# Performance work log

Hardware: AMD Instinct MI355X
Metric: run time of the kernel (lower is better)

## Reference

```python
import jax, jax.numpy as jnp
import numpy as np

N, D, H, O, E, K = 16384, 512, 512, 64, 8, 2


def _layernorm(x, g, b, eps=1e-5):
    mu = jnp.mean(x, axis=-1, keepdims=True)
    var = jnp.var(x, axis=-1, keepdims=True)
    return (x - mu) * jax.lax.rsqrt(var + eps) * g + b


def _gelu(x):
    return jax.nn.gelu(x, approximate=False)  # torch nn.GELU default (erf)


def setup_inputs() -> dict:
    key = jax.random.key(0)
    ks = jax.random.split(key, 20)
    s = 0.02
    return {
        "x": jax.random.normal(ks[0], (N, D), jnp.float32),
        # gate: Linear(D,H) -> LN(H) -> GELU -> Linear(H,E)
        "g_w1": jax.random.normal(ks[1], (D, H), jnp.float32) * s,
        "g_b1": jnp.zeros((H,), jnp.float32),
        "g_ln_g": jnp.ones((H,), jnp.float32),
        "g_ln_b": jnp.zeros((H,), jnp.float32),
        "g_w2": jax.random.normal(ks[2], (H, E), jnp.float32) * s,
        "g_b2": jnp.zeros((E,), jnp.float32),
        # experts (stacked over E): Linear(D,H)+LN+GELU, Linear(H,H)+LN+GELU, Linear(H,O)
        "e_w1": jax.random.normal(ks[3], (E, D, H), jnp.float32) * s,
        "e_b1": jnp.zeros((E, H), jnp.float32),
        "e_ln1_g": jnp.ones((E, H), jnp.float32),
        "e_ln1_b": jnp.zeros((E, H), jnp.float32),
        "e_w2": jax.random.normal(ks[4], (E, H, H), jnp.float32) * s,
        "e_b2": jnp.zeros((E, H), jnp.float32),
        "e_ln2_g": jnp.ones((E, H), jnp.float32),
        "e_ln2_b": jnp.zeros((E, H), jnp.float32),
        "e_w3": jax.random.normal(ks[5], (E, H, O), jnp.float32) * s,
        "e_b3": jnp.zeros((E, O), jnp.float32),
        # output projection Linear(O,O)
        "p_w": jax.random.normal(ks[6], (O, O), jnp.float32) * s,
        "p_b": jnp.zeros((O,), jnp.float32),
    }


def reference(x, g_w1, g_b1, g_ln_g, g_ln_b, g_w2, g_b2,
              e_w1, e_b1, e_ln1_g, e_ln1_b, e_w2, e_b2, e_ln2_g, e_ln2_b,
              e_w3, e_b3, p_w, p_b):
    n = x.shape[0]
    # --- gate ---
    gh = _gelu(_layernorm(x @ g_w1 + g_b1, g_ln_g, g_ln_b))
    gate_logits = gh @ g_w2 + g_b2                      # [N, E]
    gate_weights = jax.nn.softmax(gate_logits, axis=-1)
    top_k_weights, top_k_indices = jax.lax.top_k(gate_weights, K)
    top_k_weights = top_k_weights / jnp.sum(top_k_weights, axis=-1, keepdims=True)
    # dense per-token expert weights [N, E] (sum of top-k weights routed to each expert)
    w_dense = jnp.zeros((n, e_w1.shape[0]), x.dtype).at[
        jnp.arange(n)[:, None], top_k_indices].add(top_k_weights)
    # --- all experts on all tokens (faithful to dense loop) ---
    h1 = _gelu(_layernorm(jnp.einsum('nd,edh->enh', x, e_w1) + e_b1[:, None, :],
                          e_ln1_g[:, None, :], e_ln1_b[:, None, :]))
    h2 = _gelu(_layernorm(jnp.einsum('enh,ehk->enk', h1, e_w2) + e_b2[:, None, :],
                          e_ln2_g[:, None, :], e_ln2_b[:, None, :]))
    expert_out = jnp.einsum('enh,eho->eno', h2, e_w3) + e_b3[:, None, :]  # [E, N, O]
    combined = jnp.einsum('ne,eno->no', w_dense, expert_out)              # [N, O]
    output = combined @ p_w + p_b
    expert_usage = jnp.mean(gate_weights, axis=0)
    return (output, gate_weights, top_k_indices, top_k_weights, expert_usage)
```

## Files before the change

kernel.cpp:

```cpp
#include <hip/hip_runtime.h>
#include <hip/hip_bf16.h>

#define N_TOK 16384
#define MAX_SLOTS 33280
#define MAX_BLOCKS 520

typedef __attribute__((ext_vector_type(8))) short bf16x8;
typedef __attribute__((ext_vector_type(4))) float f32x4;
typedef unsigned short u16;

__device__ __forceinline__ u16 f2bf(float f) {
  __hip_bfloat16 h = __float2bfloat16(f);
  union { __hip_bfloat16 b; u16 u; } c; c.b = h; return c.u;
}
__device__ __forceinline__ float bfbits2f(u16 u) {
  return __uint_as_float(((unsigned)u) << 16);
}
__device__ __forceinline__ float gelu_erf(float x) {
  return 0.5f * x * (1.0f + erff(x * 0.70710678118654752f));
}
__device__ __forceinline__ float gelu_fast(float x) {
  float u = x * (0.79788456f + 0.035677408f * x * x);
  float ex;
  asm("v_exp_f32 %0, %1" : "=v"(ex) : "v"(-2.8853901f * u));
  float den = 1.0f + ex;
  float r;
  asm("v_rcp_f32 %0, %1" : "=v"(r) : "v"(den));
  return x * r;
}
__device__ __forceinline__ void gload16(const u16* g, char* lds) {
  __builtin_amdgcn_global_load_lds(
      (const __attribute__((address_space(1))) void*)g,
      (__attribute__((address_space(3))) void*)lds, 16, 0, 0);
}

__global__ __launch_bounds__(256) void prep_x(const float* __restrict__ x,
                                              u16* __restrict__ xbf,
                                              u16* __restrict__ xlo) {
  size_t i = (size_t)blockIdx.x * 256 + threadIdx.x;
  float4 v = ((const float4*)x)[i];
  float a[4] = {v.x, v.y, v.z, v.w};
  union { u16 us[4]; unsigned long long ll; } hb, lb;
#pragma unroll
  for (int j = 0; j < 4; ++j) {
    u16 hu = f2bf(a[j]);
    hb.us[j] = hu;
    lb.us[j] = f2bf(a[j] - bfbits2f(hu));
  }
  *(unsigned long long*)(xbf + i * 4) = hb.ll;
  *(unsigned long long*)(xlo + i * 4) = lb.ll;
}

template <int C>
__global__ __launch_bounds__(256) void pack_w(const float* __restrict__ src,
                                              u16* __restrict__ dst, int R) {
  __shared__ float tl[64][65];
  const int e = blockIdx.z;
  const int k0 = blockIdx.x * 64, n0 = blockIdx.y * 64;
  const float* s = src + (size_t)e * R * C;
  const int tr = threadIdx.x >> 2;
  const int tc4 = (threadIdx.x & 3) * 16;
#pragma unroll
  for (int j = 0; j < 4; ++j) {
    float4 v = *(const float4*)(s + (size_t)(k0 + tr) * C + n0 + tc4 + j * 4);
    tl[tr][tc4 + j * 4 + 0] = v.x;
    tl[tr][tc4 + j * 4 + 1] = v.y;
    tl[tr][tc4 + j * 4 + 2] = v.z;
    tl[tr][tc4 + j * 4 + 3] = v.w;
  }
  __syncthreads();
  const int nl = threadIdx.x >> 2;
  const int kl = (threadIdx.x & 3) * 16;
  const int n = n0 + nl;
  const int sx = (n >> 1) & 3;
  const int t = (k0 + kl) >> 5;
  const int q0 = ((k0 + kl) & 31) >> 3;
#pragma unroll
  for (int c = 0; c < 2; ++c) {
    int q = q0 + c;
    int p = q ^ sx;
    union { u16 us[8]; unsigned long long ll[2]; } o;
#pragma unroll
    for (int j = 0; j < 8; ++j) o.us[j] = f2bf(tl[kl + c * 8 + j][nl]);
    u16* d = dst + (((size_t)e * (R / 32) + t) * C + n) * 32 + p * 8;
    ((unsigned long long*)d)[0] = o.ll[0];
    ((unsigned long long*)d)[1] = o.ll[1];
  }
}

__global__ __launch_bounds__(256) void prep_wcat(const float* __restrict__ gw1,
                                                 u16* __restrict__ wp) {
  int idx = blockIdx.x * 256 + threadIdx.x;
  int p = idx & 3;
  int n = (idx >> 2) & 511;
  int t = idx >> 11;
  int q = p ^ ((n >> 1) & 3);
  int k0 = t * 32 + q * 8;
  union { u16 us[8]; unsigned long long ll[2]; } o;
#pragma unroll
  for (int j = 0; j < 8; ++j) {
    int k = k0 + j;
    u16 v;
    if (k < 512) {
      v = f2bf(gw1[k * 512 + n]);
    } else if (k < 1024) {
      float w = gw1[(k - 512) * 512 + n];
      v = f2bf(w - bfbits2f(f2bf(w)));
    } else {
      v = f2bf(gw1[(k - 1024) * 512 + n]);
    }
    o.us[j] = v;
  }
  unsigned long long* d = (unsigned long long*)(wp + (size_t)idx * 8);
  d[0] = o.ll[0];
  d[1] = o.ll[1];
}

__global__ __launch_bounds__(256) void prep_w2t(const float* __restrict__ gw2,
                                                float* __restrict__ w2t) {
  int i = blockIdx.x * 256 + threadIdx.x;
  int e = i >> 9, k = i & 511;
  w2t[i] = gw2[k * 8 + e];
}

template <int ROUTED, int GATHER, int LNOUT, int FAST>
__global__ __launch_bounds__(512, 4) void gemm_core(
    const u16* __restrict__ A, const u16* __restrict__ A2,
    const u16* __restrict__ Wp, long w_estride, int klen, long osplit,
    const float* __restrict__ bias, int b_estride,
    const float* __restrict__ lng, const float* __restrict__ lnb,
    u16* __restrict__ outb, float* __restrict__ outf,
    const int* __restrict__ slot_token, const int* __restrict__ blk_e,
    const int* __restrict__ blk_tok0) {
  constexpr int ABYTES = 4096;
  constexpr int BUF = ABYTES + 32768;
  constexpr int TSU = 16384;
  extern __shared__ char smem[];

  const int tid = threadIdx.x;
  const int lane = tid & 63;
  const int wv = tid >> 6;
  const int wn = wv * 64;
  const int l15 = lane & 15;
  const int lk = lane >> 4;
  const int swzk16 = (lk ^ ((l15 >> 1) & 3)) << 4;

  int e, row0, kt0, kbase;
  if (ROUTED) {
    e = blk_e[blockIdx.x];
    if (e < 0) return;
    row0 = blk_tok0[blockIdx.x];
    kt0 = 0; kbase = 0;
  } else {
    e = 0;
    row0 = blockIdx.x * 64;
    kbase = blockIdx.y * klen;
    kt0 = kbase >> 5;
  }
  const u16* We = Wp + (size_t)e * w_estride;

  const int lrq = lane >> 2;
  const int cse = (((lane & 3) ^ ((lane >> 3) & 3)) << 3);
  size_t off[5];
  int ldsoff[5], typ[5];
#pragma unroll
  for (int i = 0; i < 5; ++i) {
    int id = wv + 8 * i;
    if (id >= 36) { typ[i] = 2; off[i] = 0; ldsoff[i] = 0; continue; }
    if (id < 4) {
      int lr = id * 16 + lrq;
      long grow = GATHER ? (long)slot_token[row0 + lr] : (long)(row0 + lr);
      off[i] = (size_t)grow * 512 + cse;
      ldsoff[i] = id * 1024 + lane * 16;
      typ[i] = 0;
    } else {
      int bg = id - 4;
      off[i] = (size_t)bg * 512 + lane * 8;
      ldsoff[i] = ABYTES + bg * 1024 + lane * 16;
      typ[i] = 1;
    }
  }

  auto STAGE = [&](int t, char* b) {
    const int kg = kbase + t * 32;
    const u16* Aseg = A;
    int kc = kg;
    if (A2) {
      if (kg >= 1024) { Aseg = A2; kc = kg - 1024; }
      else if (kg >= 512) kc = kg - 512;
    }
    const u16* Bt = We + (size_t)(kt0 + t) * TSU;
#pragma unroll
    for (int i = 0; i < 5; ++i) {
      if (typ[i] == 0)      gload16(Aseg + off[i] + kc, b + ldsoff[i]);
      else if (typ[i] == 1) gload16(Bt + off[i], b + ldsoff[i]);
    }
  };

  f32x4 acc[4][4];
#pragma unroll
  for (int i = 0; i < 4; ++i)
#pragma unroll
    for (int j = 0; j < 4; ++j) acc[i][j] = (f32x4){0.f, 0.f, 0.f, 0.f};

  const int nt = klen / 32;
  char* buf0 = smem;
  char* buf1 = smem + BUF;

  STAGE(0, buf0);
  __syncthreads();
  for (int t = 0; t < nt; ++t) {
    char* cur = (t & 1) ? buf1 : buf0;
    char* nxt = (t & 1) ? buf0 : buf1;
    if (t + 1 < nt) STAGE(t + 1, nxt);
    char* cB = cur + ABYTES;
    bf16x8 af[4];
#pragma unroll
    for (int fm = 0; fm < 4; ++fm)
      af[fm] = *(const bf16x8*)(cur + (fm * 16 + l15) * 64 + swzk16);
#pragma unroll
    for (int fn = 0; fn < 4; ++fn) {
      bf16x8 bv = *(const bf16x8*)(cB + (wn + fn * 16 + l15) * 64 + swzk16);
#pragma unroll
      for (int fm = 0; fm < 4; ++fm)
        acc[fm][fn] = __builtin_amdgcn_mfma_f32_16x16x32_bf16(
            af[fm], bv, acc[fm][fn], 0, 0, 0);
    }
    __syncthreads();
  }

  if constexpr (LNOUT) {
    const float* be = bias + (size_t)e * b_estride;
    const float* ge = lng + (size_t)e * b_estride;
    const float* bbe = lnb + (size_t)e * b_estride;
    float bias_v[4], g_v[4], b_v[4];
#pragma unroll
    for (int fn = 0; fn < 4; ++fn) {
      int col = wn + fn * 16 + l15;
      bias_v[fn] = be[col]; g_v[fn] = ge[col]; b_v[fn] = bbe[col];
    }
#pragma unroll
    for (int fm = 0; fm < 4; ++fm)
#pragma unroll
      for (int fn = 0; fn < 4; ++fn)
#pragma unroll
        for (int r = 0; r < 4; ++r) acc[fm][fn][r] += bias_v[fn];

    float* redS1 = (float*)smem;
    float* redS2 = redS1 + 8 * 64;
#pragma unroll
    for (int fm = 0; fm < 4; ++fm)
#pragma unroll
      for (int r = 0; r < 4; ++r) {
        float a1 = 0.f, a2 = 0.f;
#pragma unroll
        for (int fn = 0; fn < 4; ++fn) {
          float v = acc[fm][fn][r];
          a1 += v; a2 += v * v;
        }
#pragma unroll
        for (int m = 1; m < 16; m <<= 1) {
          a1 += __shfl_xor(a1, m, 64);
          a2 += __shfl_xor(a2, m, 64);
        }
        if (l15 == 0) {
          int row = fm * 16 + lk * 4 + r;
          redS1[wv * 64 + row] = a1;
          redS2[wv * 64 + row] = a2;
        }
      }
    __syncthreads();
#pragma unroll
    for (int fm = 0; fm < 4; ++fm)
#pragma unroll
      for (int r = 0; r < 4; ++r) {
        int row = fm * 16 + lk * 4 + r;
        float S1 = 0.f, S2 = 0.f;
#pragma unroll
        for (int q = 0; q < 8; ++q) {
          S1 += redS1[q * 64 + row];
          S2 += redS2[q * 64 + row];
        }
        float mu = S1 * (1.0f / 512.0f);
        float var = S2 * (1.0f / 512.0f) - mu * mu;
        float rs = rsqrtf(var + 1e-5f);
        size_t rowg = (size_t)(row0 + row);
#pragma unroll
        for (int fn = 0; fn < 4; ++fn) {
          int col = wn + fn * 16 + l15;
          float v = (acc[fm][fn][r] - mu) * rs * g_v[fn] + b_v[fn];
          v = FAST ? gelu_fast(v) : gelu_erf(v);
          outb[rowg * 512 + col] = f2bf(v);
        }
      }
  } else {
    float* dst = outf + (size_t)blockIdx.y * osplit;
#pragma unroll
    for (int fm = 0; fm < 4; ++fm)
#pragma unroll
      for (int r = 0; r < 4; ++r) {
        size_t rowg = (size_t)(row0 + fm * 16 + lk * 4 + r);
#pragma unroll
        for (int fn = 0; fn < 4; ++fn)
          dst[rowg * 512 + wn + fn * 16 + l15] = acc[fm][fn][r];
      }
  }
}

__global__ __launch_bounds__(256) void gate2_topk(
    const float* __restrict__ gh0, const float* __restrict__ gh1,
    const float* __restrict__ b1, const float* __restrict__ lng,
    const float* __restrict__ lnb, const float* __restrict__ w2t,
    const float* __restrict__ b2, float* __restrict__ gwout,
    float* __restrict__ idxout, float* __restrict__ tkwout) {
  const int lane = threadIdx.x & 63;
  const int wv = threadIdx.x >> 6;
  const int t = blockIdx.x * 4 + wv;
  const int c0 = lane * 8;
  float v[8];
  {
    float4 a0 = *(const float4*)(gh0 + (size_t)t * 512 + c0);
    float4 a1 = *(const float4*)(gh0 + (size_t)t * 512 + c0 + 4);
    float4 h0 = *(const float4*)(gh1 + (size_t)t * 512 + c0);
    float4 h1 = *(const float4*)(gh1 + (size_t)t * 512 + c0 + 4);
    float4 bb0 = *(const float4*)(b1 + c0);
    float4 bb1 = *(const float4*)(b1 + c0 + 4);
    v[0] = a0.x + h0.x + bb0.x; v[1] = a0.y + h0.y + bb0.y;
    v[2] = a0.z + h0.z + bb0.z; v[3] = a0.w + h0.w + bb0.w;
    v[4] = a1.x + h1.x + bb1.x; v[5] = a1.y + h1.y + bb1.y;
    v[6] = a1.z + h1.z + bb1.z; v[7] = a1.w + h1.w + bb1.w;
  }
  float s1 = 0.f, s2 = 0.f;
#pragma unroll
  for (int j = 0; j < 8; ++j) { s1 += v[j]; s2 += v[j] * v[j]; }
#pragma unroll
  for (int m = 1; m < 64; m <<= 1) {
    s1 += __shfl_xor(s1, m, 64);
    s2 += __shfl_xor(s2, m, 64);
  }
  float mu = s1 * (1.0f / 512.0f);
  float var = s2 * (1.0f / 512.0f) - mu * mu;
  float rs = rsqrtf(var + 1e-5f);
  float y[8];
  {
    float4 g0 = *(const float4*)(lng + c0);
    float4 g1 = *(const float4*)(lng + c0 + 4);
    float4 q0 = *(const float4*)(lnb + c0);
    float4 q1 = *(const float4*)(lnb + c0 + 4);
    float gg[8] = {g0.x, g0.y, g0.z, g0.w, g1.x, g1.y, g1.z, g1.w};
    float qq[8] = {q0.x, q0.y, q0.z, q0.w, q1.x, q1.y, q1.z, q1.w};
#pragma unroll
    for (int j = 0; j < 8; ++j)
      y[j] = gelu_erf((v[j] - mu) * rs * gg[j] + qq[j]);
  }
  float logit[8];
#pragma unroll
  for (int e = 0; e < 8; ++e) {
    const float4* wr = (const float4*)(w2t + e * 512 + c0);
    float4 w0 = wr[0], w1 = wr[1];
    float p = y[0] * w0.x + y[1] * w0.y + y[2] * w0.z + y[3] * w0.w +
              y[4] * w1.x + y[5] * w1.y + y[6] * w1.z + y[7] * w1.w;
#pragma unroll
    for (int m = 1; m < 64; m <<= 1) p += __shfl_xor(p, m, 64);
    logit[e] = p + b2[e];
  }
  if (lane == 0) {
    float mx = logit[0];
#pragma unroll
    for (int e = 1; e < 8; ++e) mx = fmaxf(mx, logit[e]);
    float w[8], ssum = 0.f;
#pragma unroll
    for (int e = 0; e < 8; ++e) { w[e] = expf(logit[e] - mx); ssum += w[e]; }
    float inv = 1.0f / ssum;
#pragma unroll
    for (int e = 0; e < 8; ++e) w[e] *= inv;
    float w1v = -1.f, w2v = -1.f; int i1 = 0, i2 = 0;
#pragma unroll
    for (int e = 0; e < 8; ++e) {
      float vv = w[e];
      if (vv > w1v)      { w2v = w1v; i2 = i1; w1v = vv; i1 = e; }
      else if (vv > w2v) { w2v = vv; i2 = e; }
    }
    float s = w1v + w2v;
#pragma unroll
    for (int e = 0; e < 8; ++e) gwout[t * 8 + e] = w[e];
    idxout[t * 2] = (float)i1; idxout[t * 2 + 1] = (float)i2;
    tkwout[t * 2] = w1v / s;   tkwout[t * 2 + 1] = w2v / s;
  }
}

__global__ __launch_bounds__(256) void usage_k(const float* __restrict__ gw,
                                               float* __restrict__ usage) {
  __shared__ float r[256];
  int e = blockIdx.x;
  float s = 0.f;
  for (int t = threadIdx.x; t < N_TOK; t += 256) s += gw[t * 8 + e];
  r[threadIdx.x] = s;
  __syncthreads();
  for (int st = 128; st > 0; st >>= 1) {
    if (threadIdx.x < st) r[threadIdx.x] += r[threadIdx.x + st];
    __syncthreads();
  }
  if (threadIdx.x == 0) usage[e] = r[0] * (1.0f / (float)N_TOK);
}

__global__ __launch_bounds__(256) void count_hist(const float* __restrict__ idxout,
                                                  int* __restrict__ blk_cnt) {
  __shared__ int h[8];
  if (threadIdx.x < 8) h[threadIdx.x] = 0;
  __syncthreads();
  int t = blockIdx.x * 256 + threadIdx.x;
  int e0 = (int)idxout[t * 2], e1 = (int)idxout[t * 2 + 1];
  atomicAdd(&h[e0], 1);
  atomicAdd(&h[e1], 1);
  __syncthreads();
  if (threadIdx.x < 8) blk_cnt[blockIdx.x * 8 + threadIdx.x] = h[threadIdx.x];
}

__global__ __launch_bounds__(512) void k_offsets2(
    const int* __restrict__ blk_cnt, int* __restrict__ sbase,
    int* __restrict__ blk_e, int* __restrict__ blk_tok0) {
  __shared__ int cnt[64][8];
  __shared__ int ecnt[8];
  __shared__ int offs[8];
  const int tid = threadIdx.x;
  cnt[tid >> 3][tid & 7] = blk_cnt[tid];
  __syncthreads();
  if (tid < 8) {
    int s = 0;
    for (int b = 0; b < 64; ++b) s += cnt[b][tid];
    ecnt[tid] = s;
  }
  __syncthreads();
  if (tid == 0) {
    int off = 0;
    for (int e = 0; e < 8; ++e) {
      offs[e] = off;
      off += ((ecnt[e] + 63) >> 6) << 6;
    }
  }
  __syncthreads();
  {
    int b = tid >> 3, e = tid & 7;
    int s = offs[e];
    for (int bp = 0; bp < b; ++bp) s += cnt[bp][e];
    sbase[tid] = s;
  }
  for (int b = tid; b < MAX_BLOCKS; b += 512) {
    int acc = 0, be = -1, bt = 0;
#pragma unroll
    for (int e = 0; e < 8; ++e) {
      int nbe = (ecnt[e] + 63) >> 6;
      if (b >= acc && b < acc + nbe) { be = e; bt = offs[e] + (b - acc) * 64; }
      acc += nbe;
    }
    blk_e[b] = be;
    blk_tok0[b] = bt;
  }
}

__global__ __launch_bounds__(256) void k_padinit(int* __restrict__ slot_token,
                                                 float* __restrict__ slot_w) {
  int i = blockIdx.x * 256 + threadIdx.x;
  if (i < MAX_SLOTS) { slot_token[i] = 0; slot_w[i] = 0.f; }
}

__global__ __launch_bounds__(256) void k_scatter2(
    const float* __restrict__ idxout, const float* __restrict__ tkwout,
    const int* __restrict__ sbase, int* __restrict__ slot_token,
    float* __restrict__ slot_w, int* __restrict__ tok_slot) {
  __shared__ int lpos[8];
  if (threadIdx.x < 8) lpos[threadIdx.x] = 0;
  __syncthreads();
  int t = blockIdx.x * 256 + threadIdx.x;
#pragma unroll
  for (int k = 0; k < 2; ++k) {
    int e = (int)idxout[t * 2 + k];
    int lr = atomicAdd(&lpos[e], 1);
    int s = sbase[blockIdx.x * 8 + e] + lr;
    slot_token[s] = t;
    slot_w[s] = tkwout[t * 2 + k];
    tok_slot[t * 2 + k] = s;
  }
}

__global__ __launch_bounds__(256) void gemm3_eo(
    const u16* __restrict__ h, const u16* __restrict__ w3p,
    const float* __restrict__ b3, const float* __restrict__ slot_w,
    const int* __restrict__ blk_e, const int* __restrict__ blk_tok0,
    float* __restrict__ eo) {
  __shared__ char smem[2][8192];
  int e = blk_e[blockIdx.x];
  if (e < 0) return;
  int row0 = blk_tok0[blockIdx.x];

  const int tid = threadIdx.x;
  const int lane = tid & 63;
  const int wv = tid >> 6;
  const int l15 = lane & 15, lk = lane >> 4;
  const int swzk16 = (lk ^ ((l15 >> 1) & 3)) << 4;
  const u16* we = w3p + (size_t)e * 32768;

  const int lrq = lane >> 2;
  const int cse = (((lane & 3) ^ ((lane >> 3) & 3)) << 3);
  size_t aoff = (size_t)(row0 + wv * 16 + lrq) * 512 + cse;
  size_t boff = (size_t)wv * 512 + lane * 8;
  const int ldsA = wv * 1024 + lane * 16;
  const int ldsB = 4096 + wv * 1024 + lane * 16;

  auto STAGE = [&](int t, char* b) {
    gload16(h + aoff + t * 32, b + ldsA);
    gload16(we + (size_t)t * 2048 + boff, b + ldsB);
  };

  f32x4 acc[4];
#pragma unroll
  for (int j = 0; j < 4; ++j) acc[j] = (f32x4){0.f, 0.f, 0.f, 0.f};

  STAGE(0, smem[0]);
  __syncthreads();
  for (int t = 0; t < 16; ++t) {
    char* cur = smem[t & 1];
    if (t + 1 < 16) STAGE(t + 1, smem[(t + 1) & 1]);
    char* cB = cur + 4096;
    bf16x8 a = *(const bf16x8*)(cur + (wv * 16 + l15) * 64 + swzk16);
#pragma unroll
    for (int fn = 0; fn < 4; ++fn) {
      bf16x8 bv = *(const bf16x8*)(cB + (fn * 16 + l15) * 64 + swzk16);
      acc[fn] = __builtin_amdgcn_mfma_f32_16x16x32_bf16(a, bv, acc[fn], 0, 0, 0);
    }
    __syncthreads();
  }

#pragma unroll
  for (int r = 0; r < 4; ++r) {
    int row = wv * 16 + lk * 4 + r;
    float w = slot_w[row0 + row];
#pragma unroll
    for (int fn = 0; fn < 4; ++fn) {
      int col = fn * 16 + l15;
      eo[(size_t)(row0 + row) * 64 + col] = w * (acc[fn][r] + b3[e * 64 + col]);
    }
  }
}

__global__ __launch_bounds__(256) void combine_proj(
    const float* __restrict__ eo, const int* __restrict__ tok_slot,
    const float* __restrict__ pw, const float* __restrict__ pb,
    float* __restrict__ outp) {
  __shared__ float cs[64][68];
  __shared__ float pws[64][68];
  const int t0 = blockIdx.x * 64;
  const int tq = threadIdx.x & 3;
  const int tt = threadIdx.x >> 2;
#pragma unroll
  for (int j = 0; j < 4; ++j) {
    float4 v = *(const float4*)(pw + tt * 64 + tq * 16 + j * 4);
    *(float4*)&pws[tt][tq * 16 + j * 4] = v;
  }
  {
    int t = t0 + tt;
    int s1 = tok_slot[t * 2], s2 = tok_slot[t * 2 + 1];
#pragma unroll
    for (int j = 0; j < 4; ++j) {
      float4 a = *(const float4*)(eo + (size_t)s1 * 64 + tq * 16 + j * 4);
      float4 b = *(const float4*)(eo + (size_t)s2 * 64 + tq * 16 + j * 4);
      float4 c = {a.x + b.x, a.y + b.y, a.z + b.z, a.w + b.w};
      *(float4*)&cs[tt][tq * 16 + j * 4] = c;
    }
  }
  __syncthreads();
  float o[16];
#pragma unroll
  for (int i = 0; i < 16; ++i) o[i] = 0.f;
  for (int j = 0; j < 64; ++j) {
    float c = cs[tt][j];
#pragma unroll
    for (int q4 = 0; q4 < 4; ++q4) {
      float4 p = *(const float4*)&pws[j][tq * 16 + q4 * 4];
      o[q4 * 4 + 0] += c * p.x;
      o[q4 * 4 + 1] += c * p.y;
      o[q4 * 4 + 2] += c * p.z;
      o[q4 * 4 + 3] += c * p.w;
    }
  }
#pragma unroll
  for (int i = 0; i < 16; ++i)
    outp[(size_t)(t0 + tt) * 64 + tq * 16 + i] = o[i] + pb[tq * 16 + i];
}

extern "C" void kernel_launch(void* const* d_in, const int* in_sizes, int n_in,
                              void* d_out, int out_size, void* d_ws, size_t ws_size,
                              hipStream_t stream) {
  const float* x      = (const float*)d_in[0];
  const float* g_w1   = (const float*)d_in[1];
  const float* g_b1   = (const float*)d_in[2];
  const float* g_lng  = (const float*)d_in[3];
  const float* g_lnb  = (const float*)d_in[4];
  const float* g_w2   = (const float*)d_in[5];
  const float* g_b2   = (const float*)d_in[6];
  const float* e_w1   = (const float*)d_in[7];
  const float* e_b1   = (const float*)d_in[8];
  const float* e_ln1g = (const float*)d_in[9];
  const float* e_ln1b = (const float*)d_in[10];
  const float* e_w2   = (const float*)d_in[11];
  const float* e_b2   = (const float*)d_in[12];
  const float* e_ln2g = (const float*)d_in[13];
  const float* e_ln2b = (const float*)d_in[14];
  const float* e_w3   = (const float*)d_in[15];
  const float* e_b3   = (const float*)d_in[16];
  const float* p_w    = (const float*)d_in[17];
  const float* p_b    = (const float*)d_in[18];

  char* ws = (char*)d_ws;
  u16*   x_bf  = (u16*)(ws);
  u16*   x_lo  = (u16*)(ws + (16ull << 20));
  u16*   e_w1p = (u16*)(ws + (32ull << 20));
  u16*   e_w2p = (u16*)(ws + (36ull << 20));
  u16*   e_w3p = (u16*)(ws + (40ull << 20));
  u16*   wcat  = (u16*)(ws + (41ull << 20));
  float* w2t   = (float*)(ws + (43ull << 20));
  float* gh0   = (float*)(ws + (44ull << 20));
  float* gh1   = (float*)(ws + (76ull << 20));
  u16*   h     = (u16*)(ws + (44ull << 20));
  float* eo    = (float*)(ws + (112ull << 20));
  int*   slot_token = (int*)(ws + (121ull << 20));
  float* slot_w     = (float*)(ws + (121ull << 20) + (1ull << 18));
  int*   tok_slot   = (int*)(ws + (121ull << 20) + (2ull << 18));
  int*   blk_cnt    = (int*)(ws + (122ull << 20));
  int*   sbase      = blk_cnt + 512;
  int*   blk_e      = blk_cnt + 1024;
  int*   blk_tok0   = blk_cnt + 2048;
  if (ws_size < (123ull << 20)) return;

  float* fout = (float*)d_out;
  float* o_output = fout;
  float* o_gatew  = fout + 1048576;
  float* o_idx    = fout + 1179648;
  float* o_topw   = fout + 1212416;
  float* o_usage  = fout + 1245184;

  (void)hipFuncSetAttribute((const void*)gemm_core<0, 0, 0, 0>,
                            hipFuncAttributeMaxDynamicSharedMemorySize, 73728);
  (void)hipFuncSetAttribute((const void*)gemm_core<1, 1, 1, 1>,
                            hipFuncAttributeMaxDynamicSharedMemorySize, 73728);
  (void)hipFuncSetAttribute((const void*)gemm_core<1, 0, 1, 1>,
                            hipFuncAttributeMaxDynamicSharedMemorySize, 73728);

  prep_x<<<8192, 256, 0, stream>>>(x, x_bf, x_lo);
  pack_w<512><<<dim3(8, 8, 8), 256, 0, stream>>>(e_w1, e_w1p, 512);
  pack_w<512><<<dim3(8, 8, 8), 256, 0, stream>>>(e_w2, e_w2p, 512);
  pack_w<64><<<dim3(8, 1, 8), 256, 0, stream>>>(e_w3, e_w3p, 512);
  prep_wcat<<<384, 256, 0, stream>>>(g_w1, wcat);
  prep_w2t<<<16, 256, 0, stream>>>(g_w2, w2t);

  gemm_core<0, 0, 0, 0><<<dim3(256, 2), 512, 73728, stream>>>(
      x_bf, x_lo, wcat, 0, 768, (long)N_TOK * 512, nullptr, 0,
      nullptr, nullptr, nullptr, gh0, nullptr, nullptr, nullptr);
  gate2_topk<<<N_TOK / 4, 256, 0, stream>>>(gh0, gh1, g_b1, g_lng, g_lnb,
                                            w2t, g_b2, o_gatew, o_idx, o_topw);
  usage_k<<<8, 256, 0, stream>>>(o_gatew, o_usage);

  count_hist<<<64, 256, 0, stream>>>(o_idx, blk_cnt);
  k_offsets2<<<1, 512, 0, stream>>>(blk_cnt, sbase, blk_e, blk_tok0);
  k_padinit<<<(MAX_SLOTS + 255) / 256, 256, 0, stream>>>(slot_token, slot_w);
  k_scatter2<<<64, 256, 0, stream>>>(o_idx, o_topw, sbase, slot_token, slot_w,
                                     tok_slot);

  gemm_core<1, 1, 1, 1><<<MAX_BLOCKS, 512, 73728, stream>>>(
      x_bf, nullptr, e_w1p, 512 * 512, 512, 0, e_b1, 512,
      e_ln1g, e_ln1b, h, nullptr, slot_token, blk_e, blk_tok0);
  gemm_core<1, 0, 1, 1><<<MAX_BLOCKS, 512, 73728, stream>>>(
      h, nullptr, e_w2p, 512 * 512, 512, 0, e_b2, 512,
      e_ln2g, e_ln2b, h, nullptr, slot_token, blk_e, blk_tok0);
  gemm3_eo<<<MAX_BLOCKS, 256, 0, stream>>>(h, e_w3p, e_b3, slot_w, blk_e,
                                           blk_tok0, eo);
  combine_proj<<<N_TOK / 64, 256, 0, stream>>>(eo, tok_slot, p_w, p_b, o_output);
}
```

Measured before the change: 235.3 us.

## Enlarge GEMM row tiles to 128/160 with 2x4 warp grid and fewer routed blocks

Templates gemm_core on FM so the block tile covers FM*32 rows, with warps split 2x4 (M by N) and each warp computing FM x 8 MFMA fragments. The routed expert GEMMs use 160-row tiles, padding per-expert segments to 160 and cutting MAX_BLOCKS to 216, and gemm3_eo is reworked to 512 threads over 160-row tiles. The aim is more weight reuse per block and fewer blocks than the 256-CU count. The cost is more padding work, lower occupancy (launch bounds 512,2) and higher register and LDS pressure.

```diff
diff --git a/kernel.cpp b/kernel.cpp
--- a/kernel.cpp
+++ b/kernel.cpp
@@ -2,8 +2,8 @@
 #include <hip/hip_bf16.h>
 
 #define N_TOK 16384
-#define MAX_SLOTS 33280
-#define MAX_BLOCKS 520
+#define MAX_SLOTS 34080
+#define MAX_BLOCKS 216
 
 typedef __attribute__((ext_vector_type(8))) short bf16x8;
 typedef __attribute__((ext_vector_type(4))) float f32x4;
@@ -123,8 +123,8 @@
   w2t[i] = gw2[k * 8 + e];
 }
 
-template <int ROUTED, int GATHER, int LNOUT, int FAST>
-__global__ __launch_bounds__(512, 4) void gemm_core(
+template <int FM, int ROUTED, int GATHER, int LNOUT, int FAST>
+__global__ __launch_bounds__(512, 2) void gemm_core(
     const u16* __restrict__ A, const u16* __restrict__ A2,
     const u16* __restrict__ Wp, long w_estride, int klen, long osplit,
     const float* __restrict__ bias, int b_estride,
@@ -132,15 +132,20 @@
     u16* __restrict__ outb, float* __restrict__ outf,
     const int* __restrict__ slot_token, const int* __restrict__ blk_e,
     const int* __restrict__ blk_tok0) {
-  constexpr int ABYTES = 4096;
+  constexpr int BM = FM * 32;
+  constexpr int AG = FM * 2;
+  constexpr int ABYTES = BM * 64;
   constexpr int BUF = ABYTES + 32768;
+  constexpr int NL = AG + 32;
+  constexpr int L = (NL + 7) / 8;
   constexpr int TSU = 16384;
   extern __shared__ char smem[];
 
   const int tid = threadIdx.x;
   const int lane = tid & 63;
   const int wv = tid >> 6;
-  const int wn = wv * 64;
+  const int wm = (wv & 1) * (FM * 16);
+  const int wn = (wv >> 1) * 128;
   const int l15 = lane & 15;
   const int lk = lane >> 4;
   const int swzk16 = (lk ^ ((l15 >> 1) & 3)) << 4;
@@ -153,7 +158,7 @@
     kt0 = 0; kbase = 0;
   } else {
     e = 0;
-    row0 = blockIdx.x * 64;
+    row0 = blockIdx.x * BM;
     kbase = blockIdx.y * klen;
     kt0 = kbase >> 5;
   }
@@ -161,20 +166,20 @@
 
   const int lrq = lane >> 2;
   const int cse = (((lane & 3) ^ ((lane >> 3) & 3)) << 3);
-  size_t off[5];
-  int ldsoff[5], typ[5];
-#pragma unroll
-  for (int i = 0; i < 5; ++i) {
+  size_t off[L];
+  int ldsoff[L], typ[L];
+#pragma unroll
+  for (int i = 0; i < L; ++i) {
     int id = wv + 8 * i;
-    if (id >= 36) { typ[i] = 2; off[i] = 0; ldsoff[i] = 0; continue; }
-    if (id < 4) {
+    if (id >= NL) { typ[i] = 2; off[i] = 0; ldsoff[i] = 0; continue; }
+    if (id < AG) {
       int lr = id * 16 + lrq;
       long grow = GATHER ? (long)slot_token[row0 + lr] : (long)(row0 + lr);
       off[i] = (size_t)grow * 512 + cse;
       ldsoff[i] = id * 1024 + lane * 16;
       typ[i] = 0;
     } else {
-      int bg = id - 4;
+      int bg = id - AG;
       off[i] = (size_t)bg * 512 + lane * 8;
       ldsoff[i] = ABYTES + bg * 1024 + lane * 16;
       typ[i] = 1;
@@ -191,17 +196,17 @@
     }
     const u16* Bt = We + (size_t)(kt0 + t) * TSU;
 #pragma unroll
-    for (int i = 0; i < 5; ++i) {
+    for (int i = 0; i < L; ++i) {
       if (typ[i] == 0)      gload16(Aseg + off[i] + kc, b + ldsoff[i]);
       else if (typ[i] == 1) gload16(Bt + off[i], b + ldsoff[i]);
     }
   };
 
-  f32x4 acc[4][4];
-#pragma unroll
-  for (int i = 0; i < 4; ++i)
-#pragma unroll
-    for (int j = 0; j < 4; ++j) acc[i][j] = (f32x4){0.f, 0.f, 0.f, 0.f};
+  f32x4 acc[FM][8];
+#pragma unroll
+  for (int i = 0; i < FM; ++i)
+#pragma unroll
+    for (int j = 0; j < 8; ++j) acc[i][j] = (f32x4){0.f, 0.f, 0.f, 0.f};
 
   const int nt = klen / 32;
   char* buf0 = smem;
@@ -214,15 +219,15 @@
     char* nxt = (t & 1) ? buf0 : buf1;
     if (t + 1 < nt) STAGE(t + 1, nxt);
     char* cB = cur + ABYTES;
-    bf16x8 af[4];
-#pragma unroll
-    for (int fm = 0; fm < 4; ++fm)
-      af[fm] = *(const bf16x8*)(cur + (fm * 16 + l15) * 64 + swzk16);
-#pragma unroll
-    for (int fn = 0; fn < 4; ++fn) {
+    bf16x8 af[FM];
+#pragma unroll
+    for (int fm = 0; fm < FM; ++fm)
+      af[fm] = *(const bf16x8*)(cur + (wm + fm * 16 + l15) * 64 + swzk16);
+#pragma unroll
+    for (int fn = 0; fn < 8; ++fn) {
       bf16x8 bv = *(const bf16x8*)(cB + (wn + fn * 16 + l15) * 64 + swzk16);
 #pragma unroll
-      for (int fm = 0; fm < 4; ++fm)
+      for (int fm = 0; fm < FM; ++fm)
         acc[fm][fn] = __builtin_amdgcn_mfma_f32_16x16x32_bf16(
             af[fm], bv, acc[fm][fn], 0, 0, 0);
     }
@@ -233,28 +238,29 @@
     const float* be = bias + (size_t)e * b_estride;
     const float* ge = lng + (size_t)e * b_estride;
     const float* bbe = lnb + (size_t)e * b_estride;
-    float bias_v[4], g_v[4], b_v[4];
-#pragma unroll
-    for (int fn = 0; fn < 4; ++fn) {
+    float bias_v[8], g_v[8], b_v[8];
+#pragma unroll
+    for (int fn = 0; fn < 8; ++fn) {
       int col = wn + fn * 16 + l15;
       bias_v[fn] = be[col]; g_v[fn] = ge[col]; b_v[fn] = bbe[col];
     }
 #pragma unroll
-    for (int fm = 0; fm < 4; ++fm)
-#pragma unroll
-      for (int fn = 0; fn < 4; ++fn)
+    for (int fm = 0; fm < FM; ++fm)
+#pragma unroll
+      for (int fn = 0; fn < 8; ++fn)
 #pragma unroll
         for (int r = 0; r < 4; ++r) acc[fm][fn][r] += bias_v[fn];
 
     float* redS1 = (float*)smem;
-    float* redS2 = redS1 + 8 * 64;
-#pragma unroll
-    for (int fm = 0; fm < 4; ++fm)
+    float* redS2 = redS1 + 4 * BM;
+    const int g = wv >> 1;
+#pragma unroll
+    for (int fm = 0; fm < FM; ++fm)
 #pragma unroll
       for (int r = 0; r < 4; ++r) {
         float a1 = 0.f, a2 = 0.f;
 #pragma unroll
-        for (int fn = 0; fn < 4; ++fn) {
+        for (int fn = 0; fn < 8; ++fn) {
           float v = acc[fm][fn][r];
           a1 += v; a2 += v * v;
         }
@@ -264,29 +270,29 @@
           a2 += __shfl_xor(a2, m, 64);
         }
         if (l15 == 0) {
-          int row = fm * 16 + lk * 4 + r;
-          redS1[wv * 64 + row] = a1;
-          redS2[wv * 64 + row] = a2;
+          int row = wm + fm * 16 + lk * 4 + r;
+          redS1[g * BM + row] = a1;
+          redS2[g * BM + row] = a2;
         }
       }
     __syncthreads();
 #pragma unroll
-    for (int fm = 0; fm < 4; ++fm)
+    for (int fm = 0; fm < FM; ++fm)
 #pragma unroll
       for (int r = 0; r < 4; ++r) {
-        int row = fm * 16 + lk * 4 + r;
+        int row = wm + fm * 16 + lk * 4 + r;
         float S1 = 0.f, S2 = 0.f;
 #pragma unroll
-        for (int q = 0; q < 8; ++q) {
-          S1 += redS1[q * 64 + row];
-          S2 += redS2[q * 64 + row];
+        for (int q = 0; q < 4; ++q) {
+          S1 += redS1[q * BM + row];
+          S2 += redS2[q * BM + row];
         }
         float mu = S1 * (1.0f / 512.0f);
         float var = S2 * (1.0f / 512.0f) - mu * mu;
         float rs = rsqrtf(var + 1e-5f);
         size_t rowg = (size_t)(row0 + row);
 #pragma unroll
-        for (int fn = 0; fn < 4; ++fn) {
+        for (int fn = 0; fn < 8; ++fn) {
           int col = wn + fn * 16 + l15;
           float v = (acc[fm][fn][r] - mu) * rs * g_v[fn] + b_v[fn];
           v = FAST ? gelu_fast(v) : gelu_erf(v);
@@ -296,12 +302,12 @@
   } else {
     float* dst = outf + (size_t)blockIdx.y * osplit;
 #pragma unroll
-    for (int fm = 0; fm < 4; ++fm)
+    for (int fm = 0; fm < FM; ++fm)
 #pragma unroll
       for (int r = 0; r < 4; ++r) {
-        size_t rowg = (size_t)(row0 + fm * 16 + lk * 4 + r);
-#pragma unroll
-        for (int fn = 0; fn < 4; ++fn)
+        size_t rowg = (size_t)(row0 + wm + fm * 16 + lk * 4 + r);
+#pragma unroll
+        for (int fn = 0; fn < 8; ++fn)
           dst[rowg * 512 + wn + fn * 16 + l15] = acc[fm][fn][r];
       }
   }
@@ -436,7 +442,7 @@
     int off = 0;
     for (int e = 0; e < 8; ++e) {
       offs[e] = off;
-      off += ((ecnt[e] + 63) >> 6) << 6;
+      off += ((ecnt[e] + 159) / 160) * 160;
     }
   }
   __syncthreads();
@@ -450,8 +456,8 @@
     int acc = 0, be = -1, bt = 0;
 #pragma unroll
     for (int e = 0; e < 8; ++e) {
-      int nbe = (ecnt[e] + 63) >> 6;
-      if (b >= acc && b < acc + nbe) { be = e; bt = offs[e] + (b - acc) * 64; }
+      int nbe = (ecnt[e] + 159) / 160;
+      if (b >= acc && b < acc + nbe) { be = e; bt = offs[e] + (b - acc) * 160; }
       acc += nbe;
     }
     blk_e[b] = be;
@@ -484,12 +490,14 @@
   }
 }
 
-__global__ __launch_bounds__(256) void gemm3_eo(
+__global__ __launch_bounds__(512) void gemm3_eo(
     const u16* __restrict__ h, const u16* __restrict__ w3p,
     const float* __restrict__ b3, const float* __restrict__ slot_w,
     const int* __restrict__ blk_e, const int* __restrict__ blk_tok0,
     float* __restrict__ eo) {
-  __shared__ char smem[2][8192];
+  constexpr int ABYTES = 10240;
+  constexpr int BUF = ABYTES + 4096;
+  __shared__ char smem[2][BUF];
   int e = blk_e[blockIdx.x];
   if (e < 0) return;
   int row0 = blk_tok0[blockIdx.x];
@@ -497,51 +505,68 @@
   const int tid = threadIdx.x;
   const int lane = tid & 63;
   const int wv = tid >> 6;
+  const int wm = (wv & 1) * 80;
+  const int wn = (wv >> 1) * 16;
   const int l15 = lane & 15, lk = lane >> 4;
   const int swzk16 = (lk ^ ((l15 >> 1) & 3)) << 4;
   const u16* we = w3p + (size_t)e * 32768;
 
   const int lrq = lane >> 2;
   const int cse = (((lane & 3) ^ ((lane >> 3) & 3)) << 3);
-  size_t aoff = (size_t)(row0 + wv * 16 + lrq) * 512 + cse;
-  size_t boff = (size_t)wv * 512 + lane * 8;
-  const int ldsA = wv * 1024 + lane * 16;
-  const int ldsB = 4096 + wv * 1024 + lane * 16;
+  size_t off[2];
+  int ldsoff[2], typ[2];
+#pragma unroll
+  for (int i = 0; i < 2; ++i) {
+    int id = wv + 8 * i;
+    if (id >= 14) { typ[i] = 2; off[i] = 0; ldsoff[i] = 0; continue; }
+    if (id < 10) {
+      off[i] = (size_t)(row0 + id * 16 + lrq) * 512 + cse;
+      ldsoff[i] = id * 1024 + lane * 16;
+      typ[i] = 0;
+    } else {
+      int bg = id - 10;
+      off[i] = (size_t)bg * 512 + lane * 8;
+      ldsoff[i] = ABYTES + bg * 1024 + lane * 16;
+      typ[i] = 1;
+    }
+  }
 
   auto STAGE = [&](int t, char* b) {
-    gload16(h + aoff + t * 32, b + ldsA);
-    gload16(we + (size_t)t * 2048 + boff, b + ldsB);
+#pragma unroll
+    for (int i = 0; i < 2; ++i) {
+      if (typ[i] == 0)      gload16(h + off[i] + t * 32, b + ldsoff[i]);
+      else if (typ[i] == 1) gload16(we + (size_t)t * 2048 + off[i], b + ldsoff[i]);
+    }
   };
 
-  f32x4 acc[4];
-#pragma unroll
-  for (int j = 0; j < 4; ++j) acc[j] = (f32x4){0.f, 0.f, 0.f, 0.f};
+  f32x4 acc[5];
+#pragma unroll
+  for (int j = 0; j < 5; ++j) acc[j] = (f32x4){0.f, 0.f, 0.f, 0.f};
 
   STAGE(0, smem[0]);
   __syncthreads();
   for (int t = 0; t < 16; ++t) {
     char* cur = smem[t & 1];
     if (t + 1 < 16) STAGE(t + 1, smem[(t + 1) & 1]);
-    char* cB = cur + 4096;
-    bf16x8 a = *(const bf16x8*)(cur + (wv * 16 + l15) * 64 + swzk16);
-#pragma unroll
-    for (int fn = 0; fn < 4; ++fn) {
-      bf16x8 bv = *(const bf16x8*)(cB + (fn * 16 + l15) * 64 + swzk16);
-      acc[fn] = __builtin_amdgcn_mfma_f32_16x16x32_bf16(a, bv, acc[fn], 0, 0, 0);
+    char* cB = cur + ABYTES;
+    bf16x8 bv = *(const bf16x8*)(cB + (wn + l15) * 64 + swzk16);
+#pragma unroll
+    for (int fm = 0; fm < 5; ++fm) {
+      bf16x8 a = *(const bf16x8*)(cur + (wm + fm * 16 + l15) * 64 + swzk16);
+      acc[fm] = __builtin_amdgcn_mfma_f32_16x16x32_bf16(a, bv, acc[fm], 0, 0, 0);
     }
     __syncthreads();
   }
 
 #pragma unroll
-  for (int r = 0; r < 4; ++r) {
-    int row = wv * 16 + lk * 4 + r;
-    float w = slot_w[row0 + row];
-#pragma unroll
-    for (int fn = 0; fn < 4; ++fn) {
-      int col = fn * 16 + l15;
-      eo[(size_t)(row0 + row) * 64 + col] = w * (acc[fn][r] + b3[e * 64 + col]);
-    }
-  }
+  for (int fm = 0; fm < 5; ++fm)
+#pragma unroll
+    for (int r = 0; r < 4; ++r) {
+      int row = wm + fm * 16 + lk * 4 + r;
+      float w = slot_w[row0 + row];
+      int col = wn + l15;
+      eo[(size_t)(row0 + row) * 64 + col] = w * (acc[fm][r] + b3[e * 64 + col]);
+    }
 }
 
 __global__ __launch_bounds__(256) void combine_proj(
@@ -640,12 +665,12 @@
   float* o_topw   = fout + 1212416;
   float* o_usage  = fout + 1245184;
 
-  (void)hipFuncSetAttribute((const void*)gemm_core<0, 0, 0, 0>,
-                            hipFuncAttributeMaxDynamicSharedMemorySize, 73728);
-  (void)hipFuncSetAttribute((const void*)gemm_core<1, 1, 1, 1>,
-                            hipFuncAttributeMaxDynamicSharedMemorySize, 73728);
-  (void)hipFuncSetAttribute((const void*)gemm_core<1, 0, 1, 1>,
-                            hipFuncAttributeMaxDynamicSharedMemorySize, 73728);
+  (void)hipFuncSetAttribute((const void*)gemm_core<4, 0, 0, 0, 0>,
+                            hipFuncAttributeMaxDynamicSharedMemorySize, 81920);
+  (void)hipFuncSetAttribute((const void*)gemm_core<5, 1, 1, 1, 1>,
+                            hipFuncAttributeMaxDynamicSharedMemorySize, 86016);
+  (void)hipFuncSetAttribute((const void*)gemm_core<5, 1, 0, 1, 1>,
+                            hipFuncAttributeMaxDynamicSharedMemorySize, 86016);
 
   prep_x<<<8192, 256, 0, stream>>>(x, x_bf, x_lo);
   pack_w<512><<<dim3(8, 8, 8), 256, 0, stream>>>(e_w1, e_w1p, 512);
@@ -654,7 +679,7 @@
   prep_wcat<<<384, 256, 0, stream>>>(g_w1, wcat);
   prep_w2t<<<16, 256, 0, stream>>>(g_w2, w2t);
 
-  gemm_core<0, 0, 0, 0><<<dim3(256, 2), 512, 73728, stream>>>(
+  gemm_core<4, 0, 0, 0, 0><<<dim3(N_TOK / 128, 2), 512, 81920, stream>>>(
       x_bf, x_lo, wcat, 0, 768, (long)N_TOK * 512, nullptr, 0,
       nullptr, nullptr, nullptr, gh0, nullptr, nullptr, nullptr);
   gate2_topk<<<N_TOK / 4, 256, 0, stream>>>(gh0, gh1, g_b1, g_lng, g_lnb,
@@ -667,13 +692,13 @@
   k_scatter2<<<64, 256, 0, stream>>>(o_idx, o_topw, sbase, slot_token, slot_w,
                                      tok_slot);
 
-  gemm_core<1, 1, 1, 1><<<MAX_BLOCKS, 512, 73728, stream>>>(
+  gemm_core<5, 1, 1, 1, 1><<<MAX_BLOCKS, 512, 86016, stream>>>(
       x_bf, nullptr, e_w1p, 512 * 512, 512, 0, e_b1, 512,
       e_ln1g, e_ln1b, h, nullptr, slot_token, blk_e, blk_tok0);
-  gemm_core<1, 0, 1, 1><<<MAX_BLOCKS, 512, 73728, stream>>>(
+  gemm_core<5, 1, 0, 1, 1><<<MAX_BLOCKS, 512, 86016, stream>>>(
       h, nullptr, e_w2p, 512 * 512, 512, 0, e_b2, 512,
       e_ln2g, e_ln2b, h, nullptr, slot_token, blk_e, blk_tok0);
-  gemm3_eo<<<MAX_BLOCKS, 256, 0, stream>>>(h, e_w3p, e_b3, slot_w, blk_e,
+  gemm3_eo<<<MAX_BLOCKS, 512, 0, stream>>>(h, e_w3p, e_b3, slot_w, blk_e,
                                            blk_tok0, eo);
   combine_proj<<<N_TOK / 64, 256, 0, stream>>>(eo, tok_slot, p_w, p_b, o_output);
 }
```

Result: faster. 208.5 us (-11.4%).
